# Kernel tuning notes

Hardware: AMD Instinct MI355X
Metric: run time of the kernel (lower is better)

The kernel has to match this reference:

```python
import jax, jax.numpy as jnp
import numpy as np

N_POL = 100000
N_TICK = 20000
N = N_POL + N_TICK
E = 1000000
POL_FEAT = 7
EMB = 128
HID = 256
OUT = 128
N_STATES = 60


def setup_inputs() -> dict:
    key = jax.random.key(0)
    ks = jax.random.split(key, 16)
    s = 0.05
    return {
        "pol_features": jax.random.normal(ks[0], (N_POL, POL_FEAT), dtype=jnp.float32),
        "state_ids": jax.random.randint(ks[1], (N_POL,), 0, N_STATES, dtype=jnp.int32),
        "edge_index": jax.random.randint(ks[2], (2, E), 0, N, dtype=jnp.int32),
        "edge_weight": jax.random.uniform(ks[3], (E,), dtype=jnp.float32),
        # parameters
        "W_proj": jax.random.normal(ks[4], (POL_FEAT, EMB), dtype=jnp.float32) * s,
        "b_proj": jnp.zeros((EMB,), dtype=jnp.float32),
        "state_emb": jax.random.normal(ks[5], (N_STATES, EMB), dtype=jnp.float32) * s,
        "emb_tick": jax.random.normal(ks[6], (N_TICK, EMB), dtype=jnp.float32) * s,
        "W1_rel": jax.random.normal(ks[7], (EMB, HID), dtype=jnp.float32) * s,
        "b1_rel": jnp.zeros((HID,), dtype=jnp.float32),
        "W1_root": jax.random.normal(ks[8], (EMB, HID), dtype=jnp.float32) * s,
        "W2_rel": jax.random.normal(ks[9], (HID, OUT), dtype=jnp.float32) * s,
        "b2_rel": jnp.zeros((OUT,), dtype=jnp.float32),
        "W2_root": jax.random.normal(ks[10], (HID, OUT), dtype=jnp.float32) * s,
    }


def _graph_conv(x, edge_index, edge_weight, W_rel, b_rel, W_root):
    # PyG GraphConv: out = lin_rel(sum_{j->i} w_ji * x_j) + lin_root(x_i)
    src, dst = edge_index[0], edge_index[1]
    msg = x[src] * edge_weight[:, None]            # [E, d]
    agg = jax.ops.segment_sum(msg, dst, num_segments=N)  # [N, d]
    return agg @ W_rel + b_rel + x @ W_root


def reference(pol_features, state_ids, edge_index, edge_weight,
              W_proj, b_proj, state_emb, emb_tick,
              W1_rel, b1_rel, W1_root, W2_rel, b2_rel, W2_root):
    # Node features: projected politician feats + state embedding, cat tick embeddings
    pol = jax.nn.relu(pol_features @ W_proj + b_proj) + state_emb[state_ids]  # [N_POL, EMB]
    x = jnp.concatenate([pol, emb_tick], axis=0)   # [N, EMB]
    h = jax.nn.relu(_graph_conv(x, edge_index, edge_weight, W1_rel, b1_rel, W1_root))
    # dropout is identity in eval mode
    out = _graph_conv(h, edge_index, edge_weight, W2_rel, b2_rel, W2_root)
    return out  # [N, OUT]
```

## Files before the change

### kernel.cpp

```cpp
#include <hip/hip_runtime.h>
#include <hip/hip_bf16.h>

typedef unsigned short u16;
using short8  = __attribute__((ext_vector_type(8))) short;
using ushort8 = __attribute__((ext_vector_type(8))) unsigned short;
using float4v = __attribute__((ext_vector_type(4))) float;

#define N_POL  100000
#define N_TICK 20000
#define NNODE  120000
#define NEDGE  1000000

static __device__ __forceinline__ float b2f(u16 u) {
    return __uint_as_float(((unsigned)u) << 16);
}
static __device__ __forceinline__ u16 f2b(float f) {
    unsigned u = __float_as_uint(f);
    unsigned r = (u + 0x7FFFu + ((u >> 16) & 1u)) >> 16;
    return (u16)r;
}
static __device__ __forceinline__ float lde(const void* p, size_t i, int f32) {
    return f32 ? ((const float*)p)[i] : b2f(((const u16*)p)[i]);
}

static __device__ __forceinline__ size_t frag_addr(int k, int n) {
    return ((size_t)((n >> 4) * 8 + (k >> 5)) * 64 + (((k >> 3) & 3) * 16 + (n & 15))) * 8
           + (k & 7);
}

static __device__ __forceinline__ void gload_lds16(const u16* g, u16* l) {
    __builtin_amdgcn_global_load_lds(
        (const __attribute__((address_space(1))) void*)g,
        (__attribute__((address_space(3))) void*)l, 16, 0, 0);
}

__global__ void detect_k(const void* __restrict__ ew, int* __restrict__ flag) {
    if (threadIdx.x == 0) {
        const u16* p = (const u16*)ew;
        int huge = 0, allz = 1;
        for (int i = 0; i < 128; i += 2) {
            u16 b = p[i];
            if (b != 0) allz = 0;
            float v = b2f(b);
            if (!(fabsf(v) <= 4.0f)) huge = 1;
        }
        *flag = huge | allz;
    }
}

__global__ __launch_bounds__(256) void build_pol(const void* __restrict__ pf,
                                                 const int* __restrict__ sid,
                                                 const void* __restrict__ Wp,
                                                 const void* __restrict__ bp,
                                                 const void* __restrict__ semb,
                                                 const int* __restrict__ flag,
                                                 u16* __restrict__ Xb) {
    const int f32 = *flag;
    int row = blockIdx.x * 2 + (threadIdx.x >> 7);
    int j = threadIdx.x & 127;
    float s = lde(bp, j, f32);
#pragma unroll
    for (int k = 0; k < 7; k++)
        s = fmaf(lde(pf, (size_t)row * 7 + k, f32), lde(Wp, k * 128 + j, f32), s);
    s = fmaxf(s, 0.f);
    s += lde(semb, (size_t)sid[row] * 128 + j, f32);
    Xb[(size_t)row * 128 + j] = f2b(s);
}

__global__ __launch_bounds__(256) void build_tick(const void* __restrict__ et,
                                                  const int* __restrict__ flag,
                                                  u16* __restrict__ Xb) {
    const int f32 = *flag;
    int idx = blockIdx.x * 256 + threadIdx.x;
    Xb[(size_t)N_POL * 128 + idx] = f2b(lde(et, idx, f32));
}

__global__ __launch_bounds__(256) void prep_wf1(const void* __restrict__ W1rel,
                                                const void* __restrict__ W1root,
                                                const int* __restrict__ flag,
                                                u16* __restrict__ Wf) {
    const int f32 = *flag;
    int idx = blockIdx.x * 256 + threadIdx.x;
    int k = idx >> 8, n = idx & 255;
    float v = (k < 128) ? lde(W1rel, (size_t)k * 256 + n, f32)
                        : lde(W1root, (size_t)(k - 128) * 256 + n, f32);
    Wf[frag_addr(k, n)] = f2b(v);
}

__global__ __launch_bounds__(256) void prep_wf2(const void* __restrict__ W2rel,
                                                const void* __restrict__ W2root,
                                                const int* __restrict__ flag,
                                                u16* __restrict__ Wf) {
    const int f32 = *flag;
    int idx = blockIdx.x * 256 + threadIdx.x;
    int k = idx >> 8, n = idx & 255;
    float v = (n < 128) ? lde(W2rel, (size_t)k * 128 + n, f32)
                        : lde(W2root, (size_t)k * 128 + (n - 128), f32);
    Wf[frag_addr(k, n)] = f2b(v);
}

__global__ __launch_bounds__(256) void hist_dst(const int* __restrict__ ei,
                                                int* __restrict__ count,
                                                int* __restrict__ rank) {
    int e = blockIdx.x * 256 + threadIdx.x;
    if (e < NEDGE) rank[e] = atomicAdd(&count[ei[NEDGE + e]], 1);
}

__global__ __launch_bounds__(256) void scan1(const int* __restrict__ count,
                                             int* __restrict__ row_tmp,
                                             int* __restrict__ bsum) {
    __shared__ int sd[256];
    int t = threadIdx.x;
    int i = blockIdx.x * 256 + t;
    int c = (i < NNODE) ? count[i] : 0;
    sd[t] = c;
    __syncthreads();
#pragma unroll
    for (int off = 1; off < 256; off <<= 1) {
        int v = (t >= off) ? sd[t - off] : 0;
        __syncthreads();
        sd[t] += v;
        __syncthreads();
    }
    if (i < NNODE) row_tmp[i] = sd[t] - c;
    if (t == 255) bsum[blockIdx.x] = sd[t];
}

__global__ __launch_bounds__(512) void scan2(int* __restrict__ bsum, int nb) {
    __shared__ int sd[512];
    int t = threadIdx.x;
    int v = (t < nb) ? bsum[t] : 0;
    sd[t] = v;
    __syncthreads();
#pragma unroll
    for (int off = 1; off < 512; off <<= 1) {
        int u = (t >= off) ? sd[t - off] : 0;
        __syncthreads();
        sd[t] += u;
        __syncthreads();
    }
    if (t < nb) bsum[t] = sd[t] - v;
}

__global__ __launch_bounds__(256) void scan3(const int* __restrict__ row_tmp,
                                             const int* __restrict__ bsum,
                                             int* __restrict__ row_start) {
    int i = blockIdx.x * 256 + threadIdx.x;
    if (i < NNODE) row_start[i] = row_tmp[i] + bsum[blockIdx.x];
    if (i == 0) row_start[NNODE] = NEDGE;
}

__global__ __launch_bounds__(256) void fill_csr(const int* __restrict__ ei,
                                                const void* __restrict__ ew,
                                                const int* __restrict__ flag,
                                                const int* __restrict__ row_start,
                                                const int* __restrict__ rank,
                                                uint2* __restrict__ epk) {
    const int f32 = *flag;
    int e = blockIdx.x * 256 + threadIdx.x;
    if (e >= NEDGE) return;
    int src = ei[e];
    int dst = ei[NEDGE + e];
    int pos = row_start[dst] + rank[e];
    uint2 pk;
    pk.x = (unsigned)src;
    pk.y = (unsigned)f2b(lde(ew, e, f32));
    epk[pos] = pk;
}

__global__ __launch_bounds__(256) void gather128(const int* __restrict__ row_start,
                                                 const uint2* __restrict__ epk,
                                                 const u16* __restrict__ S,
                                                 u16* __restrict__ agg) {
    int n = blockIdx.x * 4 + (threadIdx.x >> 6);
    int lane = threadIdx.x & 63;
    int g4 = lane >> 4;
    int l16 = lane & 15;
    int s0 = row_start[n], s1 = row_start[n + 1];
    float a[8] = {0.f, 0.f, 0.f, 0.f, 0.f, 0.f, 0.f, 0.f};
    int e = s0;
    for (; e + 8 <= s1; e += 8) {
        uint2 p0 = epk[e + g4], p1 = epk[e + 4 + g4];
        float w0 = b2f((u16)p0.y), w1 = b2f((u16)p1.y);
        ushort8 x0 = *(const ushort8*)(S + (size_t)p0.x * 128 + l16 * 8);
        ushort8 x1 = *(const ushort8*)(S + (size_t)p1.x * 128 + l16 * 8);
#pragma unroll
        for (int j = 0; j < 8; j++) {
            a[j] = fmaf(b2f(x0[j]), w0, a[j]);
            a[j] = fmaf(b2f(x1[j]), w1, a[j]);
        }
    }
    for (; e + 4 <= s1; e += 4) {
        uint2 p = epk[e + g4];
        float w = b2f((u16)p.y);
        ushort8 x = *(const ushort8*)(S + (size_t)p.x * 128 + l16 * 8);
#pragma unroll
        for (int j = 0; j < 8; j++) a[j] = fmaf(b2f(x[j]), w, a[j]);
    }
    if (e < s1) {
        int eg = e + g4;
        int valid = eg < s1;
        uint2 p = epk[valid ? eg : s0];
        float w = valid ? b2f((u16)p.y) : 0.f;
        ushort8 x = *(const ushort8*)(S + (size_t)p.x * 128 + l16 * 8);
#pragma unroll
        for (int j = 0; j < 8; j++) a[j] = fmaf(b2f(x[j]), w, a[j]);
    }
#pragma unroll
    for (int j = 0; j < 8; j++) {
        a[j] += __shfl_xor(a[j], 16);
        a[j] += __shfl_xor(a[j], 32);
    }
    if (g4 == 0) {
        ushort8 o;
#pragma unroll
        for (int j = 0; j < 8; j++) o[j] = f2b(a[j]);
        *(ushort8*)(agg + (size_t)n * 128 + l16 * 8) = o;
    }
}

__global__ __launch_bounds__(256) void gather_add(const int* __restrict__ row_start,
                                                  const uint2* __restrict__ epk,
                                                  const u16* __restrict__ T2,
                                                  const u16* __restrict__ P,
                                                  const int* __restrict__ flag,
                                                  void* __restrict__ out) {
    const int f32 = *flag;
    int n = blockIdx.x * 4 + (threadIdx.x >> 6);
    int lane = threadIdx.x & 63;
    int g4 = lane >> 4;
    int l16 = lane & 15;
    int s0 = row_start[n], s1 = row_start[n + 1];
    float a[8] = {0.f, 0.f, 0.f, 0.f, 0.f, 0.f, 0.f, 0.f};
    int e = s0;
    for (; e + 8 <= s1; e += 8) {
        uint2 p0 = epk[e + g4], p1 = epk[e + 4 + g4];
        float w0 = b2f((u16)p0.y), w1 = b2f((u16)p1.y);
        ushort8 x0 = *(const ushort8*)(T2 + (size_t)p0.x * 128 + l16 * 8);
        ushort8 x1 = *(const ushort8*)(T2 + (size_t)p1.x * 128 + l16 * 8);
#pragma unroll
        for (int j = 0; j < 8; j++) {
            a[j] = fmaf(b2f(x0[j]), w0, a[j]);
            a[j] = fmaf(b2f(x1[j]), w1, a[j]);
        }
    }
    for (; e + 4 <= s1; e += 4) {
        uint2 p = epk[e + g4];
        float w = b2f((u16)p.y);
        ushort8 x = *(const ushort8*)(T2 + (size_t)p.x * 128 + l16 * 8);
#pragma unroll
        for (int j = 0; j < 8; j++) a[j] = fmaf(b2f(x[j]), w, a[j]);
    }
    if (e < s1) {
        int eg = e + g4;
        int valid = eg < s1;
        uint2 p = epk[valid ? eg : s0];
        float w = valid ? b2f((u16)p.y) : 0.f;
        ushort8 x = *(const ushort8*)(T2 + (size_t)p.x * 128 + l16 * 8);
#pragma unroll
        for (int j = 0; j < 8; j++) a[j] = fmaf(b2f(x[j]), w, a[j]);
    }
#pragma unroll
    for (int j = 0; j < 8; j++) {
        a[j] += __shfl_xor(a[j], 16);
        a[j] += __shfl_xor(a[j], 32);
    }
    if (g4 == 0) {
        ushort8 pv = *(const ushort8*)(P + (size_t)n * 128 + l16 * 8);
        float v[8];
#pragma unroll
        for (int j = 0; j < 8; j++) v[j] = a[j] + b2f(pv[j]);
        if (f32) {
            float4 s0v, s1v;
            s0v.x = v[0]; s0v.y = v[1]; s0v.z = v[2]; s0v.w = v[3];
            s1v.x = v[4]; s1v.y = v[5]; s1v.z = v[6]; s1v.w = v[7];
            *(float4*)((float*)out + (size_t)n * 128 + l16 * 8) = s0v;
            *(float4*)((float*)out + (size_t)n * 128 + l16 * 8 + 4) = s1v;
        } else {
            ushort8 s;
#pragma unroll
            for (int j = 0; j < 8; j++) s[j] = f2b(v[j]);
            *(ushort8*)((u16*)out + (size_t)n * 128 + l16 * 8) = s;
        }
    }
}

__global__ __launch_bounds__(256) void fused_gemm(const u16* __restrict__ agg,
                                                  const u16* __restrict__ Xb,
                                                  const u16* __restrict__ Wf1,
                                                  const u16* __restrict__ Wf2,
                                                  const void* __restrict__ b1,
                                                  const void* __restrict__ b2,
                                                  u16* __restrict__ T2,
                                                  u16* __restrict__ P,
                                                  const int* __restrict__ flag,
                                                  int M) {
    const int f32 = *flag;
    __shared__ u16 LDSU[32 * 64 * 8];
    const int row0 = blockIdx.x * 64;
    const int wid = threadIdx.x >> 6;
    const int lane = threadIdx.x & 63;
    const int q = lane >> 4, lm = lane & 15;

    {
        int kqL = lane & 31;
#pragma unroll
        for (int i = 0; i < 8; i++) {
            int t = i * 4 + wid;
            int row = 2 * t + (lane >> 5);
            int kqG = kqL ^ (row & 7);
            const u16* src = (kqG < 16)
                ? agg + ((size_t)(row0 + row)) * 128 + kqG * 8
                : Xb + ((size_t)(row0 + row)) * 128 + (kqG - 16) * 8;
            gload_lds16(src, LDSU + (size_t)t * 512);
        }
    }
    __syncthreads();

    float4v acc[4][4];
#pragma unroll
    for (int i = 0; i < 4; i++)
#pragma unroll
        for (int j = 0; j < 4; j++) acc[i][j] = (float4v){0.f, 0.f, 0.f, 0.f};
#pragma unroll
    for (int kb = 0; kb < 8; kb++) {
        short8 a[4];
#pragma unroll
        for (int ti = 0; ti < 4; ti++) {
            int rl = ti * 16 + lm;
            int chunk = (kb * 4 + q) ^ (rl & 7);
            a[ti] = *(const short8*)(LDSU + (size_t)rl * 256 + chunk * 8);
        }
        short8 b[4];
#pragma unroll
        for (int tj = 0; tj < 4; tj++) {
            int nt = wid * 4 + tj;
            b[tj] = *(const short8*)(Wf1 + ((size_t)(nt * 8 + kb) * 64 + lane) * 8);
        }
#pragma unroll
        for (int ti = 0; ti < 4; ti++)
#pragma unroll
            for (int tj = 0; tj < 4; tj++)
                acc[ti][tj] = __builtin_amdgcn_mfma_f32_16x16x32_bf16(
                    a[ti], b[tj], acc[ti][tj], 0, 0, 0);
    }
    __syncthreads();

#pragma unroll
    for (int tj = 0; tj < 4; tj++) {
        int col = wid * 64 + tj * 16 + lm;
        float bv = lde(b1, col, f32);
        int kq2 = col >> 3, jj = col & 7;
#pragma unroll
        for (int ti = 0; ti < 4; ti++) {
            int rl = ti * 16 + q * 4;
#pragma unroll
            for (int r = 0; r < 4; r++) {
                float v = fmaxf(acc[ti][tj][r] + bv, 0.f);
                LDSU[((size_t)kq2 * 64 + rl + r) * 8 + jj] = f2b(v);
            }
        }
    }
    __syncthreads();

    float4v acc2[4][4];
#pragma unroll
    for (int i = 0; i < 4; i++)
#pragma unroll
        for (int j = 0; j < 4; j++) acc2[i][j] = (float4v){0.f, 0.f, 0.f, 0.f};
#pragma unroll
    for (int kb = 0; kb < 8; kb++) {
        short8 a[4];
#pragma unroll
        for (int ti = 0; ti < 4; ti++) {
            int rl = ti * 16 + lm;
            a[ti] = *(const short8*)(LDSU + ((size_t)(kb * 4 + q) * 64 + rl) * 8);
        }
        short8 b[4];
#pragma unroll
        for (int tj = 0; tj < 4; tj++) {
            int nt = wid * 4 + tj;
            b[tj] = *(const short8*)(Wf2 + ((size_t)(nt * 8 + kb) * 64 + lane) * 8);
        }
#pragma unroll
        for (int ti = 0; ti < 4; ti++)
#pragma unroll
            for (int tj = 0; tj < 4; tj++)
                acc2[ti][tj] = __builtin_amdgcn_mfma_f32_16x16x32_bf16(
                    a[ti], b[tj], acc2[ti][tj], 0, 0, 0);
    }
    __syncthreads();

#pragma unroll
    for (int tj = 0; tj < 4; tj++) {
        int col = wid * 64 + tj * 16 + lm;
        int chunk = col >> 3, jj = col & 7;
        float bv = (col < 128) ? 0.f : lde(b2, col - 128, f32);
#pragma unroll
        for (int ti = 0; ti < 4; ti++) {
#pragma unroll
            for (int r = 0; r < 4; r++) {
                int row = ti * 16 + q * 4 + r;
                int pchunk = chunk ^ (((row >> 2) & 3) << 1);
                LDSU[((size_t)row * 32 + pchunk) * 8 + jj] = f2b(acc2[ti][tj][r] + bv);
            }
        }
    }
    __syncthreads();
#pragma unroll
    for (int i = 0; i < 8; i++) {
        int g = i * 256 + threadIdx.x;
        int row = g >> 5;
        int chunk = g & 31;
        int pchunk = chunk ^ (((row >> 2) & 3) << 1);
        short8 v = *(const short8*)(LDSU + ((size_t)row * 32 + pchunk) * 8);
        int grow = row0 + row;
        int colu = chunk * 8;
        u16* dst = (colu < 128) ? (T2 + (size_t)grow * 128 + colu)
                                : (P + (size_t)grow * 128 + (colu - 128));
        *(short8*)dst = v;
    }
    (void)M;
}

extern "C" void kernel_launch(void* const* d_in, const int* in_sizes, int n_in,
                              void* d_out, int out_size, void* d_ws, size_t ws_size,
                              hipStream_t stream) {
    const void* pf     = d_in[0];
    const int*  sid    = (const int*)d_in[1];
    const int*  ei     = (const int*)d_in[2];
    const void* ew     = d_in[3];
    const void* Wp     = d_in[4];
    const void* bp     = d_in[5];
    const void* semb   = d_in[6];
    const void* et     = d_in[7];
    const void* W1rel  = d_in[8];
    const void* b1     = d_in[9];
    const void* W1root = d_in[10];
    const void* W2rel  = d_in[11];
    const void* b2     = d_in[12];
    const void* W2root = d_in[13];

    char* w = (char*)d_ws;
    u16*   agg       = (u16*)w;
    u16*   T2        = (u16*)(w + 30720000);
    u16*   P         = (u16*)(w + 61440000);
    u16*   Wf1       = (u16*)(w + 92160000);
    u16*   Wf2       = (u16*)(w + 92291072);
    uint2* epk       = (uint2*)(w + 92422144);
    int*   rank      = (int*)(w + 100422144);
    int*   row_start = (int*)(w + 104422144);
    int*   row_tmp   = (int*)(w + 104902148);
    int*   count     = (int*)(w + 105382148);
    int*   bsum      = (int*)(w + 105862148);
    int*   flag      = (int*)(w + 105866244);
    u16*   Xb        = (u16*)d_out;

    const int EB = (NEDGE + 255) / 256;
    const int NB = (NNODE + 255) / 256;
    const int GB = (NNODE + 63) / 64;

    detect_k<<<1, 64, 0, stream>>>(ew, flag);

    hipMemsetAsync(count, 0, NNODE * sizeof(int), stream);
    hist_dst<<<EB, 256, 0, stream>>>(ei, count, rank);
    scan1<<<NB, 256, 0, stream>>>(count, row_tmp, bsum);
    scan2<<<1, 512, 0, stream>>>(bsum, NB);
    scan3<<<NB, 256, 0, stream>>>(row_tmp, bsum, row_start);
    fill_csr<<<EB, 256, 0, stream>>>(ei, ew, flag, row_start, rank, epk);

    prep_wf1<<<256, 256, 0, stream>>>(W1rel, W1root, flag, Wf1);
    prep_wf2<<<256, 256, 0, stream>>>(W2rel, W2root, flag, Wf2);

    build_pol<<<N_POL / 2, 256, 0, stream>>>(pf, sid, Wp, bp, semb, flag, Xb);
    build_tick<<<(N_TICK * 128) / 256, 256, 0, stream>>>(et, flag, Xb);

    gather128<<<NNODE / 4, 256, 0, stream>>>(row_start, epk, Xb, agg);

    fused_gemm<<<GB, 256, 0, stream>>>(agg, Xb, Wf1, Wf2, b1, b2, T2, P, flag, NNODE);

    gather_add<<<NNODE / 4, 256, 0, stream>>>(row_start, epk, T2, P, flag, d_out);
}
```

Before: 379.8 us.

## Make fused GEMM persistent with double-buffered LDS prefetch; merge small prep kernels

The fused two-layer GEMM now runs as a persistent kernel with 512 blocks that loop over 64-row tiles. Each block prefetches the next tile's agg/X rows into a second LDS buffer while it computes the current tile, so global loads overlap with MFMA work. The build_pol/build_tick kernels and the two weight-prep kernels are each merged into one launch to cut launch overhead. In exchange, LDS use doubles to 64KB per block, which may lower occupancy, and the fixed grid of 512 blocks may leave the 1875 tiles unevenly spread across CUs.

Result: no change. 382.6 us (+0.7%).

```diff
diff --git a/kernel.cpp b/kernel.cpp
--- a/kernel.cpp
+++ b/kernel.cpp
@@ -10,6 +10,8 @@
 #define N_TICK 20000
 #define NNODE  120000
 #define NEDGE  1000000
+#define NTILE  1875
+#define GB2    512
 
 static __device__ __forceinline__ float b2f(u16 u) {
     return __uint_as_float(((unsigned)u) << 16);
@@ -32,6 +34,23 @@
     __builtin_amdgcn_global_load_lds(
         (const __attribute__((address_space(1))) void*)g,
         (__attribute__((address_space(3))) void*)l, 16, 0, 0);
+}
+
+static __device__ __forceinline__ void stage_tile(const u16* __restrict__ agg,
+                                                  const u16* __restrict__ Xb,
+                                                  int row0, u16* dst,
+                                                  int wid, int lane) {
+    int kqL = lane & 31;
+#pragma unroll
+    for (int i = 0; i < 8; i++) {
+        int t = i * 4 + wid;
+        int row = 2 * t + (lane >> 5);
+        int kqG = kqL ^ (row & 7);
+        const u16* src = (kqG < 16)
+            ? agg + ((size_t)(row0 + row)) * 128 + kqG * 8
+            : Xb + ((size_t)(row0 + row)) * 128 + (kqG - 16) * 8;
+        gload_lds16(src, dst + (size_t)t * 512);
+    }
 }
 
 __global__ void detect_k(const void* __restrict__ ew, int* __restrict__ flag) {
@@ -48,55 +67,51 @@
     }
 }
 
-__global__ __launch_bounds__(256) void build_pol(const void* __restrict__ pf,
-                                                 const int* __restrict__ sid,
-                                                 const void* __restrict__ Wp,
-                                                 const void* __restrict__ bp,
-                                                 const void* __restrict__ semb,
-                                                 const int* __restrict__ flag,
-                                                 u16* __restrict__ Xb) {
+__global__ __launch_bounds__(256) void build_x(const void* __restrict__ pf,
+                                               const int* __restrict__ sid,
+                                               const void* __restrict__ Wp,
+                                               const void* __restrict__ bp,
+                                               const void* __restrict__ semb,
+                                               const void* __restrict__ et,
+                                               const int* __restrict__ flag,
+                                               u16* __restrict__ Xb) {
     const int f32 = *flag;
-    int row = blockIdx.x * 2 + (threadIdx.x >> 7);
-    int j = threadIdx.x & 127;
-    float s = lde(bp, j, f32);
-#pragma unroll
-    for (int k = 0; k < 7; k++)
-        s = fmaf(lde(pf, (size_t)row * 7 + k, f32), lde(Wp, k * 128 + j, f32), s);
-    s = fmaxf(s, 0.f);
-    s += lde(semb, (size_t)sid[row] * 128 + j, f32);
-    Xb[(size_t)row * 128 + j] = f2b(s);
-}
-
-__global__ __launch_bounds__(256) void build_tick(const void* __restrict__ et,
-                                                  const int* __restrict__ flag,
-                                                  u16* __restrict__ Xb) {
+    if (blockIdx.x < N_POL / 2) {
+        int row = blockIdx.x * 2 + (threadIdx.x >> 7);
+        int j = threadIdx.x & 127;
+        float s = lde(bp, j, f32);
+#pragma unroll
+        for (int k = 0; k < 7; k++)
+            s = fmaf(lde(pf, (size_t)row * 7 + k, f32), lde(Wp, k * 128 + j, f32), s);
+        s = fmaxf(s, 0.f);
+        s += lde(semb, (size_t)sid[row] * 128 + j, f32);
+        Xb[(size_t)row * 128 + j] = f2b(s);
+    } else {
+        int idx = (blockIdx.x - N_POL / 2) * 256 + threadIdx.x;
+        Xb[(size_t)N_POL * 128 + idx] = f2b(lde(et, idx, f32));
+    }
+}
+
+__global__ __launch_bounds__(256) void prep_wf(const void* __restrict__ W1rel,
+                                               const void* __restrict__ W1root,
+                                               const void* __restrict__ W2rel,
+                                               const void* __restrict__ W2root,
+                                               const int* __restrict__ flag,
+                                               u16* __restrict__ Wf1,
+                                               u16* __restrict__ Wf2) {
     const int f32 = *flag;
     int idx = blockIdx.x * 256 + threadIdx.x;
-    Xb[(size_t)N_POL * 128 + idx] = f2b(lde(et, idx, f32));
-}
-
-__global__ __launch_bounds__(256) void prep_wf1(const void* __restrict__ W1rel,
-                                                const void* __restrict__ W1root,
-                                                const int* __restrict__ flag,
-                                                u16* __restrict__ Wf) {
-    const int f32 = *flag;
-    int idx = blockIdx.x * 256 + threadIdx.x;
-    int k = idx >> 8, n = idx & 255;
-    float v = (k < 128) ? lde(W1rel, (size_t)k * 256 + n, f32)
-                        : lde(W1root, (size_t)(k - 128) * 256 + n, f32);
-    Wf[frag_addr(k, n)] = f2b(v);
-}
-
-__global__ __launch_bounds__(256) void prep_wf2(const void* __restrict__ W2rel,
-                                                const void* __restrict__ W2root,
-                                                const int* __restrict__ flag,
-                                                u16* __restrict__ Wf) {
-    const int f32 = *flag;
-    int idx = blockIdx.x * 256 + threadIdx.x;
-    int k = idx >> 8, n = idx & 255;
-    float v = (n < 128) ? lde(W2rel, (size_t)k * 128 + n, f32)
-                        : lde(W2root, (size_t)k * 128 + (n - 128), f32);
-    Wf[frag_addr(k, n)] = f2b(v);
+    int id = idx & 65535;
+    int k = id >> 8, n = id & 255;
+    if (idx < 65536) {
+        float v = (k < 128) ? lde(W1rel, (size_t)k * 256 + n, f32)
+                            : lde(W1root, (size_t)(k - 128) * 256 + n, f32);
+        Wf1[frag_addr(k, n)] = f2b(v);
+    } else {
+        float v = (n < 128) ? lde(W2rel, (size_t)k * 128 + n, f32)
+                            : lde(W2root, (size_t)k * 128 + (n - 128), f32);
+        Wf2[frag_addr(k, n)] = f2b(v);
+    }
 }
 
 __global__ __launch_bounds__(256) void hist_dst(const int* __restrict__ ei,
@@ -294,133 +309,129 @@
                                                   u16* __restrict__ T2,
                                                   u16* __restrict__ P,
                                                   const int* __restrict__ flag,
-                                                  int M) {
+                                                  int ntiles) {
     const int f32 = *flag;
-    __shared__ u16 LDSU[32 * 64 * 8];
-    const int row0 = blockIdx.x * 64;
+    __shared__ u16 LDS2[2][16384];
     const int wid = threadIdx.x >> 6;
     const int lane = threadIdx.x & 63;
     const int q = lane >> 4, lm = lane & 15;
 
-    {
-        int kqL = lane & 31;
+    stage_tile(agg, Xb, blockIdx.x * 64, LDS2[0], wid, lane);
+
+    for (int k = 0, t = blockIdx.x; t < ntiles; k++, t += GB2) {
+        const int cur = k & 1;
+        u16* B = LDS2[cur];
+        const int row0 = t * 64;
+        __syncthreads();
+
+        float4v acc[4][4];
+#pragma unroll
+        for (int i = 0; i < 4; i++)
+#pragma unroll
+            for (int j = 0; j < 4; j++) acc[i][j] = (float4v){0.f, 0.f, 0.f, 0.f};
+#pragma unroll
+        for (int kb = 0; kb < 8; kb++) {
+            short8 a[4];
+#pragma unroll
+            for (int ti = 0; ti < 4; ti++) {
+                int rl = ti * 16 + lm;
+                int chunk = (kb * 4 + q) ^ (rl & 7);
+                a[ti] = *(const short8*)(B + (size_t)rl * 256 + chunk * 8);
+            }
+            short8 b[4];
+#pragma unroll
+            for (int tj = 0; tj < 4; tj++) {
+                int nt = wid * 4 + tj;
+                b[tj] = *(const short8*)(Wf1 + ((size_t)(nt * 8 + kb) * 64 + lane) * 8);
+            }
+#pragma unroll
+            for (int ti = 0; ti < 4; ti++)
+#pragma unroll
+                for (int tj = 0; tj < 4; tj++)
+                    acc[ti][tj] = __builtin_amdgcn_mfma_f32_16x16x32_bf16(
+                        a[ti], b[tj], acc[ti][tj], 0, 0, 0);
+        }
+        __syncthreads();
+
+#pragma unroll
+        for (int tj = 0; tj < 4; tj++) {
+            int col = wid * 64 + tj * 16 + lm;
+            float bv = lde(b1, col, f32);
+            int kq2 = col >> 3, jj = col & 7;
+#pragma unroll
+            for (int ti = 0; ti < 4; ti++) {
+                int rl = ti * 16 + q * 4;
+#pragma unroll
+                for (int r = 0; r < 4; r++) {
+                    float v = fmaxf(acc[ti][tj][r] + bv, 0.f);
+                    B[((size_t)kq2 * 64 + rl + r) * 8 + jj] = f2b(v);
+                }
+            }
+        }
+        __syncthreads();
+
+        float4v acc2[4][4];
+#pragma unroll
+        for (int i = 0; i < 4; i++)
+#pragma unroll
+            for (int j = 0; j < 4; j++) acc2[i][j] = (float4v){0.f, 0.f, 0.f, 0.f};
+#pragma unroll
+        for (int kb = 0; kb < 8; kb++) {
+            short8 a[4];
+#pragma unroll
+            for (int ti = 0; ti < 4; ti++) {
+                int rl = ti * 16 + lm;
+                a[ti] = *(const short8*)(B + ((size_t)(kb * 4 + q) * 64 + rl) * 8);
+            }
+            short8 b[4];
+#pragma unroll
+            for (int tj = 0; tj < 4; tj++) {
+                int nt = wid * 4 + tj;
+                b[tj] = *(const short8*)(Wf2 + ((size_t)(nt * 8 + kb) * 64 + lane) * 8);
+            }
+#pragma unroll
+            for (int ti = 0; ti < 4; ti++)
+#pragma unroll
+                for (int tj = 0; tj < 4; tj++)
+                    acc2[ti][tj] = __builtin_amdgcn_mfma_f32_16x16x32_bf16(
+                        a[ti], b[tj], acc2[ti][tj], 0, 0, 0);
+        }
+
+        if (t + GB2 < ntiles)
+            stage_tile(agg, Xb, (t + GB2) * 64, LDS2[cur ^ 1], wid, lane);
+
+        __syncthreads();
+
+#pragma unroll
+        for (int tj = 0; tj < 4; tj++) {
+            int col = wid * 64 + tj * 16 + lm;
+            int chunk = col >> 3, jj = col & 7;
+            float bv = (col < 128) ? 0.f : lde(b2, col - 128, f32);
+#pragma unroll
+            for (int ti = 0; ti < 4; ti++) {
+#pragma unroll
+                for (int r = 0; r < 4; r++) {
+                    int row = ti * 16 + q * 4 + r;
+                    int pchunk = chunk ^ (((row >> 2) & 3) << 1);
+                    B[((size_t)row * 32 + pchunk) * 8 + jj] = f2b(acc2[ti][tj][r] + bv);
+                }
+            }
+        }
+        __syncthreads();
 #pragma unroll
         for (int i = 0; i < 8; i++) {
-            int t = i * 4 + wid;
-            int row = 2 * t + (lane >> 5);
-            int kqG = kqL ^ (row & 7);
-            const u16* src = (kqG < 16)
-                ? agg + ((size_t)(row0 + row)) * 128 + kqG * 8
-                : Xb + ((size_t)(row0 + row)) * 128 + (kqG - 16) * 8;
-            gload_lds16(src, LDSU + (size_t)t * 512);
-        }
-    }
-    __syncthreads();
-
-    float4v acc[4][4];
-#pragma unroll
-    for (int i = 0; i < 4; i++)
-#pragma unroll
-        for (int j = 0; j < 4; j++) acc[i][j] = (float4v){0.f, 0.f, 0.f, 0.f};
-#pragma unroll
-    for (int kb = 0; kb < 8; kb++) {
-        short8 a[4];
-#pragma unroll
-        for (int ti = 0; ti < 4; ti++) {
-            int rl = ti * 16 + lm;
-            int chunk = (kb * 4 + q) ^ (rl & 7);
-            a[ti] = *(const short8*)(LDSU + (size_t)rl * 256 + chunk * 8);
-        }
-        short8 b[4];
-#pragma unroll
-        for (int tj = 0; tj < 4; tj++) {
-            int nt = wid * 4 + tj;
-            b[tj] = *(const short8*)(Wf1 + ((size_t)(nt * 8 + kb) * 64 + lane) * 8);
-        }
-#pragma unroll
-        for (int ti = 0; ti < 4; ti++)
-#pragma unroll
-            for (int tj = 0; tj < 4; tj++)
-                acc[ti][tj] = __builtin_amdgcn_mfma_f32_16x16x32_bf16(
-                    a[ti], b[tj], acc[ti][tj], 0, 0, 0);
-    }
-    __syncthreads();
-
-#pragma unroll
-    for (int tj = 0; tj < 4; tj++) {
-        int col = wid * 64 + tj * 16 + lm;
-        float bv = lde(b1, col, f32);
-        int kq2 = col >> 3, jj = col & 7;
-#pragma unroll
-        for (int ti = 0; ti < 4; ti++) {
-            int rl = ti * 16 + q * 4;
-#pragma unroll
-            for (int r = 0; r < 4; r++) {
-                float v = fmaxf(acc[ti][tj][r] + bv, 0.f);
-                LDSU[((size_t)kq2 * 64 + rl + r) * 8 + jj] = f2b(v);
-            }
-        }
-    }
-    __syncthreads();
-
-    float4v acc2[4][4];
-#pragma unroll
-    for (int i = 0; i < 4; i++)
-#pragma unroll
-        for (int j = 0; j < 4; j++) acc2[i][j] = (float4v){0.f, 0.f, 0.f, 0.f};
-#pragma unroll
-    for (int kb = 0; kb < 8; kb++) {
-        short8 a[4];
-#pragma unroll
-        for (int ti = 0; ti < 4; ti++) {
-            int rl = ti * 16 + lm;
-            a[ti] = *(const short8*)(LDSU + ((size_t)(kb * 4 + q) * 64 + rl) * 8);
-        }
-        short8 b[4];
-#pragma unroll
-        for (int tj = 0; tj < 4; tj++) {
-            int nt = wid * 4 + tj;
-            b[tj] = *(const short8*)(Wf2 + ((size_t)(nt * 8 + kb) * 64 + lane) * 8);
-        }
-#pragma unroll
-        for (int ti = 0; ti < 4; ti++)
-#pragma unroll
-            for (int tj = 0; tj < 4; tj++)
-                acc2[ti][tj] = __builtin_amdgcn_mfma_f32_16x16x32_bf16(
-                    a[ti], b[tj], acc2[ti][tj], 0, 0, 0);
-    }
-    __syncthreads();
-
-#pragma unroll
-    for (int tj = 0; tj < 4; tj++) {
-        int col = wid * 64 + tj * 16 + lm;
-        int chunk = col >> 3, jj = col & 7;
-        float bv = (col < 128) ? 0.f : lde(b2, col - 128, f32);
-#pragma unroll
-        for (int ti = 0; ti < 4; ti++) {
-#pragma unroll
-            for (int r = 0; r < 4; r++) {
-                int row = ti * 16 + q * 4 + r;
-                int pchunk = chunk ^ (((row >> 2) & 3) << 1);
-                LDSU[((size_t)row * 32 + pchunk) * 8 + jj] = f2b(acc2[ti][tj][r] + bv);
-            }
-        }
-    }
-    __syncthreads();
-#pragma unroll
-    for (int i = 0; i < 8; i++) {
-        int g = i * 256 + threadIdx.x;
-        int row = g >> 5;
-        int chunk = g & 31;
-        int pchunk = chunk ^ (((row >> 2) & 3) << 1);
-        short8 v = *(const short8*)(LDSU + ((size_t)row * 32 + pchunk) * 8);
-        int grow = row0 + row;
-        int colu = chunk * 8;
-        u16* dst = (colu < 128) ? (T2 + (size_t)grow * 128 + colu)
-                                : (P + (size_t)grow * 128 + (colu - 128));
-        *(short8*)dst = v;
-    }
-    (void)M;
+            int g = i * 256 + threadIdx.x;
+            int row = g >> 5;
+            int chunk = g & 31;
+            int pchunk = chunk ^ (((row >> 2) & 3) << 1);
+            short8 v = *(const short8*)(B + ((size_t)row * 32 + pchunk) * 8);
+            int grow = row0 + row;
+            int colu = chunk * 8;
+            u16* dst = (colu < 128) ? (T2 + (size_t)grow * 128 + colu)
+                                    : (P + (size_t)grow * 128 + (colu - 128));
+            *(short8*)dst = v;
+        }
+    }
 }
 
 extern "C" void kernel_launch(void* const* d_in, const int* in_sizes, int n_in,
@@ -458,7 +469,6 @@
 
     const int EB = (NEDGE + 255) / 256;
     const int NB = (NNODE + 255) / 256;
-    const int GB = (NNODE + 63) / 64;
 
     detect_k<<<1, 64, 0, stream>>>(ew, flag);
 
@@ -469,15 +479,14 @@
     scan3<<<NB, 256, 0, stream>>>(row_tmp, bsum, row_start);
     fill_csr<<<EB, 256, 0, stream>>>(ei, ew, flag, row_start, rank, epk);
 
-    prep_wf1<<<256, 256, 0, stream>>>(W1rel, W1root, flag, Wf1);
-    prep_wf2<<<256, 256, 0, stream>>>(W2rel, W2root, flag, Wf2);
-
-    build_pol<<<N_POL / 2, 256, 0, stream>>>(pf, sid, Wp, bp, semb, flag, Xb);
-    build_tick<<<(N_TICK * 128) / 256, 256, 0, stream>>>(et, flag, Xb);
+    prep_wf<<<512, 256, 0, stream>>>(W1rel, W1root, W2rel, W2root, flag, Wf1, Wf2);
+
+    build_x<<<N_POL / 2 + (N_TICK * 128) / 256, 256, 0, stream>>>(
+        pf, sid, Wp, bp, semb, et, flag, Xb);
 
     gather128<<<NNODE / 4, 256, 0, stream>>>(row_start, epk, Xb, agg);
 
-    fused_gemm<<<GB, 256, 0, stream>>>(agg, Xb, Wf1, Wf2, b1, b2, T2, P, flag, NNODE);
+    fused_gemm<<<GB2, 256, 0, stream>>>(agg, Xb, Wf1, Wf2, b1, b2, T2, P, flag, NTILE);
 
     gather_add<<<NNODE / 4, 256, 0, stream>>>(row_start, epk, T2, P, flag, d_out);
 }
```
